# Optimization experiments

Measured on AMD Instinct MI355X. Metric: run time of the kernel, lower is better.

## Reference

```python
import jax, jax.numpy as jnp
import numpy as np

B, C, H, W = 4, 256, 64, 64
C8 = C // 8


def setup_inputs() -> dict:
    key = jax.random.key(0)
    ks = jax.random.split(key, 9)
    s_in = 1.0 / np.sqrt(C)
    return {
        "x": jax.random.normal(ks[0], (B, C, H, W), dtype=jnp.float32),
        "Wq": jax.random.normal(ks[1], (C8, C), dtype=jnp.float32) * s_in,
        "bq": jax.random.normal(ks[2], (C8,), dtype=jnp.float32) * 0.01,
        "Wk": jax.random.normal(ks[3], (C8, C), dtype=jnp.float32) * s_in,
        "bk": jax.random.normal(ks[4], (C8,), dtype=jnp.float32) * 0.01,
        "Wv": jax.random.normal(ks[5], (C, C), dtype=jnp.float32) * s_in,
        "bv": jax.random.normal(ks[6], (C,), dtype=jnp.float32) * 0.01,
        "Wo": jax.random.normal(ks[7], (C, C), dtype=jnp.float32) * s_in,
        "bo": jax.random.normal(ks[8], (C,), dtype=jnp.float32) * 0.01,
    }


def reference(x, Wq, bq, Wk, bk, Wv, bv, Wo, bo):
    b, c, h, w = x.shape
    n = h * w
    xf = x.reshape(b, c, n)                                   # (B, C, N)
    # 1x1 convs are channel GEMMs
    q = jnp.einsum('bcn,dc->bnd', xf, Wq) + bq                # (B, N, C8)
    k = jnp.einsum('bcn,dc->bdn', xf, Wk) + bk[:, None]       # (B, C8, N)
    v = jnp.einsum('bcn,dc->bdn', xf, Wv) + bv[:, None]       # (B, C, N)
    energy = jnp.einsum('bnd,bdm->bnm', q, k)                 # (B, N, N)
    attn = jax.nn.softmax(energy, axis=-1)
    # out[b,c,i] = sum_j v[b,c,j] * attn[b,i,j]
    out = jnp.einsum('bcj,bij->bci', v, attn)                 # (B, C, N)
    out = out.reshape(b, c, h, w) + x                         # residual
    out = jnp.einsum('bchw,dc->bdhw', out, Wo) + bo[None, :, None, None]
    return out
```

## Files before the change

### kernel.cpp

```cpp
#include <hip/hip_runtime.h>

#define DEV __device__ __forceinline__

constexpr int B_  = 4;
constexpr int C_  = 256;
constexpr int C8_ = 32;
constexpr int N_  = 4096;
constexpr float LOG2E = 1.4426950408889634f;

using u16 = unsigned short;
using u32 = unsigned int;

typedef __attribute__((ext_vector_type(8))) short bf16x8;
typedef __attribute__((ext_vector_type(4))) float f32x4;

DEV float bf2f(u16 u) { return __uint_as_float(((u32)u) << 16); }
DEV u16   f2bf(float f) {
  u32 i = __float_as_uint(f);
  i += 0x7fffu + ((i >> 16) & 1u);
  return (u16)(i >> 16);
}
DEV u32 pack_rtz(float a, float b) {
  return __builtin_amdgcn_perm(__float_as_uint(b), __float_as_uint(a), 0x07060302);
}

DEV void lds_barrier() {
  asm volatile("s_waitcnt lgkmcnt(0)\n\ts_barrier" ::: "memory");
}

__global__ __launch_bounds__(256) void prep(
    const float* __restrict__ Wq, const float* __restrict__ Wk,
    const float* __restrict__ Wv, const float* __restrict__ Wo,
    const float* __restrict__ x,
    u16* __restrict__ WqH, u16* __restrict__ WqL,
    u16* __restrict__ WkH, u16* __restrict__ WkL,
    u16* __restrict__ WvH,
    u16* __restrict__ WoH, u16* __restrict__ WoL,
    u16* __restrict__ xTh, u16* __restrict__ xTl)
{
  __shared__ float tf[64][65];
  const int tid = threadIdx.x;

  if (blockIdx.x < 576) {
    int i = blockIdx.x * 256 + tid;
    if (i < 8192) {
      float v = Wq[i] * LOG2E;
      u16 h = f2bf(v); WqH[i] = h; WqL[i] = f2bf(v - bf2f(h));
    } else if (i < 16384) {
      int off = i - 8192;
      float v = Wk[off];
      u16 h = f2bf(v); WkH[off] = h; WkL[off] = f2bf(v - bf2f(h));
    } else if (i < 81920) {
      int off = i - 16384;
      WvH[off] = f2bf(Wv[off]);
    } else {
      int off = i - 81920;
      float v = Wo[off];
      u16 h = f2bf(v); WoH[off] = h; WoL[off] = f2bf(v - bf2f(h));
    }
    return;
  }

  const int lid = blockIdx.x - 576;
  const int b  = lid >> 8;
  const int c0 = ((lid >> 6) & 3) * 64;
  const int n0 = (lid & 63) * 64;
  const int nl = tid & 63, cb = tid >> 6;

  #pragma unroll
  for (int cc = 0; cc < 16; ++cc) {
    int cl = cb * 16 + cc;
    tf[nl][cl] = x[((size_t)b * C_ + c0 + cl) * N_ + n0 + nl];
  }
  __syncthreads();

  #pragma unroll
  for (int it = 0; it < 2; ++it) {
    int idx = tid + it * 256;
    int n = idx >> 3, q = idx & 7;
    u32 ph[4], pl[4];
    #pragma unroll
    for (int j = 0; j < 4; ++j) {
      float v0 = tf[n][q * 8 + 2 * j], v1 = tf[n][q * 8 + 2 * j + 1];
      u16 h0 = f2bf(v0), h1 = f2bf(v1);
      ph[j] = (u32)h0 | ((u32)h1 << 16);
      pl[j] = (u32)f2bf(v0 - bf2f(h0)) | ((u32)f2bf(v1 - bf2f(h1)) << 16);
    }
    size_t off = ((size_t)b * N_ + n0 + n) * C_ + c0 + q * 8;
    *(uint4*)&xTh[off] = make_uint4(ph[0], ph[1], ph[2], ph[3]);
    *(uint4*)&xTl[off] = make_uint4(pl[0], pl[1], pl[2], pl[3]);
  }
}

__global__ __launch_bounds__(256) void qkv_mfma(
    const u16* __restrict__ xTh, const u16* __restrict__ xTl,
    const u16* __restrict__ WqH, const u16* __restrict__ WqL,
    const u16* __restrict__ WkH, const u16* __restrict__ WkL,
    const u16* __restrict__ WvH,
    const float* __restrict__ bq, const float* __restrict__ bk,
    const float* __restrict__ bv,
    u16* __restrict__ qt, u16* __restrict__ kt, u16* __restrict__ vb)
{
  __shared__ __align__(16) u16 xsh[32][270];
  __shared__ __align__(16) u16 xsl[32][270];

  const int tid = threadIdx.x;
  const int lane = tid & 63, w = tid >> 6, m = lane & 15, quad = lane >> 4;
  const int b = blockIdx.y, n0 = blockIdx.x * 32;

  #pragma unroll
  for (int it = 0; it < 4; ++it) {
    int chunk = tid + it * 256;
    int row = chunk >> 5, col = (chunk & 31) * 8;
    size_t g = ((size_t)b * N_ + n0 + row) * C_ + col;
    *(uint4*)&xsh[row][col] = *(const uint4*)(xTh + g);
    *(uint4*)&xsl[row][col] = *(const uint4*)(xTl + g);
  }
  __syncthreads();

  const u16* qkH = (w < 2) ? (WqH + (size_t)(w * 16 + m) * C_)
                           : (WkH + (size_t)((w - 2) * 16 + m) * C_);
  const u16* qkL = (w < 2) ? (WqL + (size_t)(w * 16 + m) * C_)
                           : (WkL + (size_t)((w - 2) * 16 + m) * C_);

  f32x4 ov[4][2], oq[2];
  #pragma unroll
  for (int dt = 0; dt < 4; ++dt)
    #pragma unroll
    for (int nt = 0; nt < 2; ++nt) ov[dt][nt] = (f32x4){0.f, 0.f, 0.f, 0.f};
  #pragma unroll
  for (int nt = 0; nt < 2; ++nt) oq[nt] = (f32x4){0.f, 0.f, 0.f, 0.f};

  for (int K = 0; K < 8; ++K) {
    const int ko = K * 32 + quad * 8;
    bf16x8 xh[2], xl[2];
    #pragma unroll
    for (int nt = 0; nt < 2; ++nt) {
      xh[nt] = *(const bf16x8*)&xsh[nt * 16 + m][ko];
      xl[nt] = *(const bf16x8*)&xsl[nt * 16 + m][ko];
    }
    #pragma unroll
    for (int dt = 0; dt < 4; ++dt) {
      bf16x8 whi = *(const bf16x8*)(WvH + (size_t)(64 * w + dt * 16 + m) * C_ + ko);
      #pragma unroll
      for (int nt = 0; nt < 2; ++nt)
        ov[dt][nt] = __builtin_amdgcn_mfma_f32_16x16x32_bf16(whi, xh[nt], ov[dt][nt], 0, 0, 0);
    }
    {
      bf16x8 bhi = *(const bf16x8*)(qkH + ko);
      bf16x8 blo = *(const bf16x8*)(qkL + ko);
      #pragma unroll
      for (int nt = 0; nt < 2; ++nt) {
        oq[nt] = __builtin_amdgcn_mfma_f32_16x16x32_bf16(xh[nt], bhi, oq[nt], 0, 0, 0);
        oq[nt] = __builtin_amdgcn_mfma_f32_16x16x32_bf16(xl[nt], bhi, oq[nt], 0, 0, 0);
        oq[nt] = __builtin_amdgcn_mfma_f32_16x16x32_bf16(xh[nt], blo, oq[nt], 0, 0, 0);
      }
    }
  }

  #pragma unroll
  for (int dt = 0; dt < 4; ++dt)
    #pragma unroll
    for (int r = 0; r < 4; ++r) {
      int oc = 64 * w + dt * 16 + quad * 4 + r;
      float bias = bv[oc];
      #pragma unroll
      for (int nt = 0; nt < 2; ++nt)
        vb[((size_t)b * C_ + oc) * N_ + n0 + nt * 16 + m] = f2bf(ov[dt][nt][r] + bias);
    }
  {
    u16* qk_out = (w < 2) ? qt : kt;
    int dbase = (w & 1) * 16;
    float bias = (w < 2) ? bq[dbase + m] * LOG2E : bk[dbase + m];
    #pragma unroll
    for (int nt = 0; nt < 2; ++nt)
      #pragma unroll
      for (int r = 0; r < 4; ++r)
        qk_out[((size_t)b * N_ + n0 + nt * 16 + quad * 4 + r) * C8_ + dbase + m] =
            f2bf(oq[nt][r] + bias);
  }
}

__global__ __launch_bounds__(256) void attn_mfma(
    const u16* __restrict__ qt, const u16* __restrict__ kt,
    const u16* __restrict__ vb,
    u16* __restrict__ Onorm, float* __restrict__ ml)
{
  __shared__ __align__(16) u16  ps[2][64][136];
  __shared__ __align__(16) float als[2][64];
  __shared__ float lfin[64];

  const int tid = threadIdx.x, lane = tid & 63, w = tid >> 6;
  const int m = lane & 15, quad = lane >> 4;

  const int lid = blockIdx.x + gridDim.x * (blockIdx.y + gridDim.y * blockIdx.z);
  const int grp = lid & 15, ksl = grp & 3, b = grp >> 2;
  const int i0 = (lid >> 4) * 64;

  const bf16x8 qfrag =
      *(const bf16x8*)(qt + ((size_t)b * N_ + i0 + w * 16 + m) * C8_ + quad * 8);
  const u16* kbase = kt + (size_t)b * N_ * C8_;
  const u16* vrow  = vb + ((size_t)b * C_ + w * 64 + m) * N_;

  f32x4 o[4][4];
  #pragma unroll
  for (int t = 0; t < 4; ++t)
    #pragma unroll
    for (int ct = 0; ct < 4; ++ct) o[t][ct] = (f32x4){0.f, 0.f, 0.f, 0.f};
  float m_r = -1e30f, l_r = 0.f;

  const int jbeg = ksl * 1024, jend = jbeg + 1024;
  int buf = 0;

  for (int j0 = jbeg; j0 < jend; j0 += 128, buf ^= 1) {
    f32x4 s[8];
    bf16x8 kA[4];
    #pragma unroll
    for (int t = 0; t < 4; ++t)
      kA[t] = *(const bf16x8*)(kbase + (size_t)(j0 + t * 16 + m) * C8_ + quad * 8);
    #pragma unroll
    for (int t = 0; t < 4; ++t)
      s[t] = __builtin_amdgcn_mfma_f32_16x16x32_bf16(
          kA[t], qfrag, (f32x4){0.f, 0.f, 0.f, 0.f}, 0, 0, 0);
    bf16x8 vB[4][2];
    #pragma unroll
    for (int ct = 0; ct < 4; ++ct)
      #pragma unroll
      for (int kk = 0; kk < 2; ++kk)
        vB[ct][kk] = *(const bf16x8*)(vrow + (size_t)ct * 16 * N_ + j0 + kk * 32 + quad * 8);
    #pragma unroll
    for (int t = 0; t < 4; ++t)
      kA[t] = *(const bf16x8*)(kbase + (size_t)(j0 + (t + 4) * 16 + m) * C8_ + quad * 8);
    #pragma unroll
    for (int t = 0; t < 4; ++t)
      s[t + 4] = __builtin_amdgcn_mfma_f32_16x16x32_bf16(
          kA[t], qfrag, (f32x4){0.f, 0.f, 0.f, 0.f}, 0, 0, 0);

    float mx = -1e30f;
    #pragma unroll
    for (int t = 0; t < 8; ++t)
      #pragma unroll
      for (int r = 0; r < 4; ++r) mx = fmaxf(mx, s[t][r]);
    mx = fmaxf(mx, __shfl_xor(mx, 16));
    mx = fmaxf(mx, __shfl_xor(mx, 32));
    float mn = fmaxf(m_r, mx);
    float al = exp2f(m_r - mn);
    m_r = mn;
    float sm = 0.f;
    #pragma unroll
    for (int t = 0; t < 8; ++t)
      #pragma unroll
      for (int r = 0; r < 4; ++r) {
        s[t][r] = exp2f(s[t][r] - mn);
        sm += s[t][r];
      }
    sm += __shfl_xor(sm, 16);
    sm += __shfl_xor(sm, 32);
    l_r = l_r * al + sm;

    #pragma unroll
    for (int t = 0; t < 8; ++t)
      *(uint2*)&ps[buf][w * 16 + m][t * 16 + quad * 4] =
          make_uint2(pack_rtz(s[t][0], s[t][1]), pack_rtz(s[t][2], s[t][3]));
    if (quad == 0) als[buf][w * 16 + m] = al;

    lds_barrier();

    #pragma unroll
    for (int t = 0; t < 4; ++t) {
      float4 alv = *(const float4*)&als[buf][t * 16 + quad * 4];
      #pragma unroll
      for (int ct = 0; ct < 4; ++ct) {
        o[t][ct][0] *= alv.x; o[t][ct][1] *= alv.y;
        o[t][ct][2] *= alv.z; o[t][ct][3] *= alv.w;
      }
    }

    #pragma unroll
    for (int kk = 0; kk < 2; ++kk)
      #pragma unroll
      for (int t = 0; t < 4; ++t) {
        bf16x8 pf = *(const bf16x8*)&ps[buf][t * 16 + m][kk * 32 + quad * 8];
        #pragma unroll
        for (int ct = 0; ct < 4; ++ct)
          o[t][ct] = __builtin_amdgcn_mfma_f32_16x16x32_bf16(pf, vB[ct][kk], o[t][ct], 0, 0, 0);
      }

    __builtin_amdgcn_sched_barrier(0);

    #pragma unroll
    for (int ct = 0; ct < 4; ++ct)
      #pragma unroll
      for (int kk = 0; kk < 2; ++kk)
        vB[ct][kk] = *(const bf16x8*)(vrow + (size_t)ct * 16 * N_ + j0 + (kk + 2) * 32 + quad * 8);

    #pragma unroll
    for (int kk = 0; kk < 2; ++kk)
      #pragma unroll
      for (int t = 0; t < 4; ++t) {
        bf16x8 pf = *(const bf16x8*)&ps[buf][t * 16 + m][(kk + 2) * 32 + quad * 8];
        #pragma unroll
        for (int ct = 0; ct < 4; ++ct)
          o[t][ct] = __builtin_amdgcn_mfma_f32_16x16x32_bf16(pf, vB[ct][kk], o[t][ct], 0, 0, 0);
      }
  }

  if (quad == 0) lfin[w * 16 + m] = 1.f / l_r;
  lds_barrier();

  u16* Ob = Onorm + (((size_t)ksl * B_ + b) * N_ + i0) * C_ + w * 64;
  #pragma unroll
  for (int t = 0; t < 4; ++t) {
    float4 lv = *(const float4*)&lfin[t * 16 + quad * 4];
    float linv[4] = {lv.x, lv.y, lv.z, lv.w};
    #pragma unroll
    for (int ct = 0; ct < 4; ++ct)
      #pragma unroll
      for (int r = 0; r < 4; ++r)
        Ob[(size_t)(t * 16 + quad * 4 + r) * C_ + ct * 16 + m] = f2bf(o[t][ct][r] * linv[r]);
  }

  if (quad == 0) {
    size_t mli = ((size_t)ksl * B_ + b) * N_ + i0 + w * 16 + m;
    ml[mli] = m_r;
    ml[(size_t)4 * B_ * N_ + mli] = l_r;
  }
}

__global__ __launch_bounds__(256) void out_mfma(
    const u16* __restrict__ Onorm, const float* __restrict__ ml,
    const u16* __restrict__ xTh,
    const u16* __restrict__ WoH, const u16* __restrict__ WoL,
    const float* __restrict__ bo, float* __restrict__ out)
{
  __shared__ __align__(16) u16 hs[32][270];

  const int tid = threadIdx.x;
  const int lane = tid & 63, w = tid >> 6, m = lane & 15, quad = lane >> 4;
  const int b = blockIdx.y, n0 = blockIdx.x * 32;
  constexpr size_t BN = (size_t)B_ * N_;

  #pragma unroll
  for (int it = 0; it < 4; ++it) {
    int chunk = tid + it * 256;
    int row = chunk >> 5, col = (chunk & 31) * 8;
    size_t nrow = (size_t)b * N_ + n0 + row;

    float mm0 = ml[nrow], mm1 = ml[BN + nrow], mm2 = ml[2 * BN + nrow], mm3 = ml[3 * BN + nrow];
    float M = fmaxf(fmaxf(mm0, mm1), fmaxf(mm2, mm3));
    float ws[4];
    ws[0] = ml[4 * BN + nrow] * exp2f(mm0 - M);
    ws[1] = ml[5 * BN + nrow] * exp2f(mm1 - M);
    ws[2] = ml[6 * BN + nrow] * exp2f(mm2 - M);
    ws[3] = ml[7 * BN + nrow] * exp2f(mm3 - M);
    float inv = 1.f / (ws[0] + ws[1] + ws[2] + ws[3]);
    #pragma unroll
    for (int s = 0; s < 4; ++s) ws[s] *= inv;

    uint4 xv = *(const uint4*)(xTh + nrow * C_ + col);
    u32 xq[4] = {xv.x, xv.y, xv.z, xv.w};
    float acc[8];
    #pragma unroll
    for (int j = 0; j < 4; ++j) {
      acc[2 * j]     = bf2f((u16)(xq[j] & 0xffff));
      acc[2 * j + 1] = bf2f((u16)(xq[j] >> 16));
    }
    #pragma unroll
    for (int s = 0; s < 4; ++s) {
      uint4 ovv = *(const uint4*)(Onorm + (s * BN + nrow) * C_ + col);
      u32 oq[4] = {ovv.x, ovv.y, ovv.z, ovv.w};
      #pragma unroll
      for (int j = 0; j < 4; ++j) {
        acc[2 * j]     += ws[s] * bf2f((u16)(oq[j] & 0xffff));
        acc[2 * j + 1] += ws[s] * bf2f((u16)(oq[j] >> 16));
      }
    }
    uint4 pk;
    pk.x = (u32)f2bf(acc[0]) | ((u32)f2bf(acc[1]) << 16);
    pk.y = (u32)f2bf(acc[2]) | ((u32)f2bf(acc[3]) << 16);
    pk.z = (u32)f2bf(acc[4]) | ((u32)f2bf(acc[5]) << 16);
    pk.w = (u32)f2bf(acc[6]) | ((u32)f2bf(acc[7]) << 16);
    *(uint4*)&hs[row][col] = pk;
  }
  __syncthreads();

  f32x4 o[4][2];
  #pragma unroll
  for (int dt = 0; dt < 4; ++dt)
    #pragma unroll
    for (int nt = 0; nt < 2; ++nt) o[dt][nt] = (f32x4){0.f, 0.f, 0.f, 0.f};

  for (int K = 0; K < 8; ++K) {
    const int ko = K * 32 + quad * 8;
    bf16x8 hf[2];
    #pragma unroll
    for (int nt = 0; nt < 2; ++nt) hf[nt] = *(const bf16x8*)&hs[nt * 16 + m][ko];
    #pragma unroll
    for (int dt = 0; dt < 4; ++dt) {
      bf16x8 whi = *(const bf16x8*)(WoH + (size_t)(64 * w + dt * 16 + m) * C_ + ko);
      bf16x8 wlo = *(const bf16x8*)(WoL + (size_t)(64 * w + dt * 16 + m) * C_ + ko);
      #pragma unroll
      for (int nt = 0; nt < 2; ++nt) {
        o[dt][nt] = __builtin_amdgcn_mfma_f32_16x16x32_bf16(whi, hf[nt], o[dt][nt], 0, 0, 0);
        o[dt][nt] = __builtin_amdgcn_mfma_f32_16x16x32_bf16(wlo, hf[nt], o[dt][nt], 0, 0, 0);
      }
    }
  }

  #pragma unroll
  for (int dt = 0; dt < 4; ++dt)
    #pragma unroll
    for (int r = 0; r < 4; ++r) {
      int d = 64 * w + dt * 16 + quad * 4 + r;
      float bias = bo[d];
      #pragma unroll
      for (int nt = 0; nt < 2; ++nt)
        out[((size_t)b * C_ + d) * N_ + n0 + nt * 16 + m] = o[dt][nt][r] + bias;
    }
}

extern "C" void kernel_launch(void* const* d_in, const int* in_sizes, int n_in,
                              void* d_out, int out_size, void* d_ws, size_t ws_size,
                              hipStream_t stream)
{
  const float* x  = (const float*)d_in[0];
  const float* Wq = (const float*)d_in[1];
  const float* bq = (const float*)d_in[2];
  const float* Wk = (const float*)d_in[3];
  const float* bk = (const float*)d_in[4];
  const float* Wv = (const float*)d_in[5];
  const float* bv = (const float*)d_in[6];
  const float* Wo = (const float*)d_in[7];
  const float* bo = (const float*)d_in[8];

  u16* p = (u16*)d_ws;
  u16* qt  = p;  p += (size_t)B_ * N_ * C8_;
  u16* kt  = p;  p += (size_t)B_ * N_ * C8_;
  u16* vb  = p;  p += (size_t)B_ * C_ * N_;
  u16* xTh = p;  p += (size_t)B_ * N_ * C_;
  u16* WqH = p;  p += 8192;
  u16* WqL = p;  p += 8192;
  u16* WkH = p;  p += 8192;
  u16* WkL = p;  p += 8192;
  u16* WvH = p;  p += 65536;
  u16* WoH = p;  p += 65536;
  u16* WoL = p;  p += 65536;
  float* ml = (float*)p;  p += (size_t)16 * B_ * N_;
  u16* xTl   = p;
  u16* Onorm = p;

  float* out = (float*)d_out;

  prep<<<1600, 256, 0, stream>>>(Wq, Wk, Wv, Wo, x,
      WqH, WqL, WkH, WkL, WvH, WoH, WoL, xTh, xTl);
  qkv_mfma<<<dim3(N_ / 32, B_), 256, 0, stream>>>(
      xTh, xTl, WqH, WqL, WkH, WkL, WvH, bq, bk, bv, qt, kt, vb);
  attn_mfma<<<dim3(N_ / 64, 4, B_), 256, 0, stream>>>(qt, kt, vb, Onorm, ml);
  out_mfma<<<dim3(N_ / 32, B_), 256, 0, stream>>>(Onorm, ml, xTh, WoH, WoL, bo, out);
}
```

Baseline: 204.8 us.

## Halve attention query tile and split score computation across warp pairs

The attention kernel now handles 32 query rows per block instead of 64, doubling the grid. The QK^T score work for each 128-key chunk is split between two warp pairs, each covering 64 keys, and they combine their row maxima through LDS with an extra barrier. Per-thread accumulators shrink from 4x4 to 2x4 tiles, and launch_bounds asks for 3 blocks per CU. The aim is to lower register pressure and raise occupancy. In exchange there is an extra barrier per iteration and each block re-reads the full V tile for half as many queries, which doubles V traffic.

```diff
diff --git a/kernel.cpp b/kernel.cpp
--- a/kernel.cpp
+++ b/kernel.cpp
@@ -181,30 +181,33 @@
   }
 }
 
-__global__ __launch_bounds__(256) void attn_mfma(
+__global__ __launch_bounds__(256, 3) void attn_mfma(
     const u16* __restrict__ qt, const u16* __restrict__ kt,
     const u16* __restrict__ vb,
     u16* __restrict__ Onorm, float* __restrict__ ml)
 {
-  __shared__ __align__(16) u16  ps[2][64][136];
-  __shared__ __align__(16) float als[2][64];
-  __shared__ float lfin[64];
+  __shared__ __align__(16) u16  ps[2][32][136];
+  __shared__ __align__(16) float als[2][32];
+  __shared__ __align__(16) float pmax[2][32];
+  __shared__ __align__(16) float lsum[2][32];
 
   const int tid = threadIdx.x, lane = tid & 63, w = tid >> 6;
   const int m = lane & 15, quad = lane >> 4;
+  const int qg = w & 1, jh = w >> 1;
 
   const int lid = blockIdx.x + gridDim.x * (blockIdx.y + gridDim.y * blockIdx.z);
   const int grp = lid & 15, ksl = grp & 3, b = grp >> 2;
-  const int i0 = (lid >> 4) * 64;
+  const int i0 = (lid >> 4) * 32;
+  const int q = qg * 16 + m;
 
   const bf16x8 qfrag =
-      *(const bf16x8*)(qt + ((size_t)b * N_ + i0 + w * 16 + m) * C8_ + quad * 8);
+      *(const bf16x8*)(qt + ((size_t)b * N_ + i0 + q) * C8_ + quad * 8);
   const u16* kbase = kt + (size_t)b * N_ * C8_;
   const u16* vrow  = vb + ((size_t)b * C_ + w * 64 + m) * N_;
 
-  f32x4 o[4][4];
-  #pragma unroll
-  for (int t = 0; t < 4; ++t)
+  f32x4 o[2][4];
+  #pragma unroll
+  for (int t = 0; t < 2; ++t)
     #pragma unroll
     for (int ct = 0; ct < 4; ++ct) o[t][ct] = (f32x4){0.f, 0.f, 0.f, 0.f};
   float m_r = -1e30f, l_r = 0.f;
@@ -213,42 +216,41 @@
   int buf = 0;
 
   for (int j0 = jbeg; j0 < jend; j0 += 128, buf ^= 1) {
-    f32x4 s[8];
+    f32x4 s[4];
     bf16x8 kA[4];
     #pragma unroll
     for (int t = 0; t < 4; ++t)
-      kA[t] = *(const bf16x8*)(kbase + (size_t)(j0 + t * 16 + m) * C8_ + quad * 8);
+      kA[t] = *(const bf16x8*)(kbase + (size_t)(j0 + jh * 64 + t * 16 + m) * C8_ + quad * 8);
     #pragma unroll
     for (int t = 0; t < 4; ++t)
       s[t] = __builtin_amdgcn_mfma_f32_16x16x32_bf16(
           kA[t], qfrag, (f32x4){0.f, 0.f, 0.f, 0.f}, 0, 0, 0);
+
     bf16x8 vB[4][2];
     #pragma unroll
     for (int ct = 0; ct < 4; ++ct)
       #pragma unroll
       for (int kk = 0; kk < 2; ++kk)
         vB[ct][kk] = *(const bf16x8*)(vrow + (size_t)ct * 16 * N_ + j0 + kk * 32 + quad * 8);
+
+    float mx = -1e30f;
     #pragma unroll
     for (int t = 0; t < 4; ++t)
-      kA[t] = *(const bf16x8*)(kbase + (size_t)(j0 + (t + 4) * 16 + m) * C8_ + quad * 8);
-    #pragma unroll
-    for (int t = 0; t < 4; ++t)
-      s[t + 4] = __builtin_amdgcn_mfma_f32_16x16x32_bf16(
-          kA[t], qfrag, (f32x4){0.f, 0.f, 0.f, 0.f}, 0, 0, 0);
-
-    float mx = -1e30f;
-    #pragma unroll
-    for (int t = 0; t < 8; ++t)
       #pragma unroll
       for (int r = 0; r < 4; ++r) mx = fmaxf(mx, s[t][r]);
     mx = fmaxf(mx, __shfl_xor(mx, 16));
     mx = fmaxf(mx, __shfl_xor(mx, 32));
-    float mn = fmaxf(m_r, mx);
+    if (quad == 0) pmax[jh][q] = mx;
+
+    lds_barrier();
+
+    float mo = fmaxf(pmax[0][q], pmax[1][q]);
+    float mn = fmaxf(m_r, mo);
     float al = exp2f(m_r - mn);
     m_r = mn;
     float sm = 0.f;
     #pragma unroll
-    for (int t = 0; t < 8; ++t)
+    for (int t = 0; t < 4; ++t)
       #pragma unroll
       for (int r = 0; r < 4; ++r) {
         s[t][r] = exp2f(s[t][r] - mn);
@@ -259,15 +261,15 @@
     l_r = l_r * al + sm;
 
     #pragma unroll
-    for (int t = 0; t < 8; ++t)
-      *(uint2*)&ps[buf][w * 16 + m][t * 16 + quad * 4] =
+    for (int t = 0; t < 4; ++t)
+      *(uint2*)&ps[buf][q][jh * 64 + t * 16 + quad * 4] =
           make_uint2(pack_rtz(s[t][0], s[t][1]), pack_rtz(s[t][2], s[t][3]));
-    if (quad == 0) als[buf][w * 16 + m] = al;
+    if (quad == 0 && jh == 0) als[buf][q] = al;
 
     lds_barrier();
 
     #pragma unroll
-    for (int t = 0; t < 4; ++t) {
+    for (int t = 0; t < 2; ++t) {
       float4 alv = *(const float4*)&als[buf][t * 16 + quad * 4];
       #pragma unroll
       for (int ct = 0; ct < 4; ++ct) {
@@ -279,7 +281,7 @@
     #pragma unroll
     for (int kk = 0; kk < 2; ++kk)
       #pragma unroll
-      for (int t = 0; t < 4; ++t) {
+      for (int t = 0; t < 2; ++t) {
         bf16x8 pf = *(const bf16x8*)&ps[buf][t * 16 + m][kk * 32 + quad * 8];
         #pragma unroll
         for (int ct = 0; ct < 4; ++ct)
@@ -297,7 +299,7 @@
     #pragma unroll
     for (int kk = 0; kk < 2; ++kk)
       #pragma unroll
-      for (int t = 0; t < 4; ++t) {
+      for (int t = 0; t < 2; ++t) {
         bf16x8 pf = *(const bf16x8*)&ps[buf][t * 16 + m][(kk + 2) * 32 + quad * 8];
         #pragma unroll
         for (int ct = 0; ct < 4; ++ct)
@@ -305,14 +307,16 @@
       }
   }
 
-  if (quad == 0) lfin[w * 16 + m] = 1.f / l_r;
+  if (quad == 0) lsum[jh][q] = l_r;
   lds_barrier();
 
   u16* Ob = Onorm + (((size_t)ksl * B_ + b) * N_ + i0) * C_ + w * 64;
   #pragma unroll
-  for (int t = 0; t < 4; ++t) {
-    float4 lv = *(const float4*)&lfin[t * 16 + quad * 4];
-    float linv[4] = {lv.x, lv.y, lv.z, lv.w};
+  for (int t = 0; t < 2; ++t) {
+    float4 l0 = *(const float4*)&lsum[0][t * 16 + quad * 4];
+    float4 l1 = *(const float4*)&lsum[1][t * 16 + quad * 4];
+    float linv[4] = {1.f / (l0.x + l1.x), 1.f / (l0.y + l1.y),
+                     1.f / (l0.z + l1.z), 1.f / (l0.w + l1.w)};
     #pragma unroll
     for (int ct = 0; ct < 4; ++ct)
       #pragma unroll
@@ -320,10 +324,10 @@
         Ob[(size_t)(t * 16 + quad * 4 + r) * C_ + ct * 16 + m] = f2bf(o[t][ct][r] * linv[r]);
   }
 
-  if (quad == 0) {
-    size_t mli = ((size_t)ksl * B_ + b) * N_ + i0 + w * 16 + m;
+  if (quad == 0 && jh == 0) {
+    size_t mli = ((size_t)ksl * B_ + b) * N_ + i0 + q;
     ml[mli] = m_r;
-    ml[(size_t)4 * B_ * N_ + mli] = l_r;
+    ml[(size_t)4 * B_ * N_ + mli] = lsum[0][q] + lsum[1][q];
   }
 }
 
@@ -455,6 +459,6 @@
       WqH, WqL, WkH, WkL, WvH, WoH, WoL, xTh, xTl);
   qkv_mfma<<<dim3(N_ / 32, B_), 256, 0, stream>>>(
       xTh, xTl, WqH, WqL, WkH, WkL, WvH, bq, bk, bv, qt, kt, vb);
-  attn_mfma<<<dim3(N_ / 64, 4, B_), 256, 0, stream>>>(qt, kt, vb, Onorm, ml);
+  attn_mfma<<<dim3(N_ / 32, 4, B_), 256, 0, stream>>>(qt, kt, vb, Onorm, ml);
   out_mfma<<<dim3(N_ / 32, B_), 256, 0, stream>>>(Onorm, ml, xTh, WoH, WoL, bo, out);
 }
```

New measurement: 259.3 us. +26.6%, slower.
